# Kernel optimization log

Hardware: AMD Instinct MI355X
Metric: run time of the kernel (lower is better)

Reference implementation:

```python
import jax, jax.numpy as jnp
import numpy as np

N = 50000
E = 600000
C = 128          # out_channels (== in_channels)
L = 3            # num_conv layers
HID = 32
NUM_CLASSES = 7


def setup_inputs() -> dict:
    key = jax.random.key(0)
    ks = jax.random.split(key, 16)
    bound = 1.0 / np.sqrt(C)
    inp = {
        "x": jax.random.normal(ks[0], (N, C), dtype=jnp.float32),
        "edge_index": jax.random.randint(ks[1], (2, E), 0, N, dtype=jnp.int32),
        "edge_weight": jax.random.uniform(ks[2], (E,), dtype=jnp.float32),
        # GatedGraphConv weight: [num_layers, C, C], uniform(-1/sqrt(C), 1/sqrt(C))
        "conv_weight": jax.random.uniform(ks[3], (L, C, C), minval=-bound, maxval=bound, dtype=jnp.float32),
        # GRUCell params (torch layout: [3C, C] for ih and hh, gate order r,z,n)
        "w_ih": jax.random.uniform(ks[4], (3 * C, C), minval=-bound, maxval=bound, dtype=jnp.float32),
        "w_hh": jax.random.uniform(ks[5], (3 * C, C), minval=-bound, maxval=bound, dtype=jnp.float32),
        "b_ih": jax.random.uniform(ks[6], (3 * C,), minval=-bound, maxval=bound, dtype=jnp.float32),
        "b_hh": jax.random.uniform(ks[7], (3 * C,), minval=-bound, maxval=bound, dtype=jnp.float32),
        # MLP: C -> 32 -> 32 -> 32 -> NUM_CLASSES, tanh between hidden layers
        "w0": jax.random.normal(ks[8], (HID, C), dtype=jnp.float32) * 0.05,
        "b0": jnp.zeros((HID,), dtype=jnp.float32),
        "w1": jax.random.normal(ks[9], (HID, HID), dtype=jnp.float32) * 0.1,
        "b1": jnp.zeros((HID,), dtype=jnp.float32),
        "w2": jax.random.normal(ks[10], (HID, HID), dtype=jnp.float32) * 0.1,
        "b2": jnp.zeros((HID,), dtype=jnp.float32),
        "w3": jax.random.normal(ks[11], (NUM_CLASSES, HID), dtype=jnp.float32) * 0.1,
        "b3": jnp.zeros((NUM_CLASSES,), dtype=jnp.float32),
    }
    return inp


def _gru_cell(m, h, w_ih, w_hh, b_ih, b_hh):
    # torch GRUCell: gates ordered (r, z, n)
    gx = m @ w_ih.T + b_ih          # [N, 3C]
    gh = h @ w_hh.T + b_hh          # [N, 3C]
    xr, xz, xn = jnp.split(gx, 3, axis=-1)
    hr, hz, hn = jnp.split(gh, 3, axis=-1)
    r = jax.nn.sigmoid(xr + hr)
    z = jax.nn.sigmoid(xz + hz)
    n = jnp.tanh(xn + r * hn)
    return (1.0 - z) * n + z * h


def reference(x, edge_index, edge_weight, conv_weight, w_ih, w_hh, b_ih, b_hh,
              w0, b0, w1, b1, w2, b2, w3, b3):
    src, dst = edge_index[0], edge_index[1]
    h = x  # in_channels == out_channels, no padding needed
    for i in range(L):
        m = h @ conv_weight[i]                          # [N, C] dense GEMM
        msgs = edge_weight[:, None] * m[src]            # gather + edge weighting [E, C]
        agg = jax.ops.segment_sum(msgs, dst, num_segments=N)  # scatter-add [N, C]
        h = _gru_cell(agg, h, w_ih, w_hh, b_ih, b_hh)
    # MLP with tanh between hidden layers, linear last
    y = jnp.tanh(h @ w0.T + b0)
    y = jnp.tanh(y @ w1.T + b1)
    y = jnp.tanh(y @ w2.T + b2)
    y = y @ w3.T + b3
    return jax.nn.log_softmax(y, axis=-1)
```

## Files before the change

kernel.cpp:

```cpp
#include <hip/hip_runtime.h>
#include <hip/hip_bf16.h>
#include <math.h>

#define NN 50000
#define NE 600000
#define CC 128
#define NL 3
#define NRG (NN / 16)
#define C_RG 4
#define G_RG 4
#define SCAN_B 196

typedef __attribute__((ext_vector_type(8))) short bf16x8;
typedef __attribute__((ext_vector_type(4))) float f32x4;
typedef unsigned short ushort_t;
typedef unsigned int uint_t;

__device__ inline ushort_t f2bf(float f) {
    __hip_bfloat16 b = __float2bfloat16(f);
    return *reinterpret_cast<ushort_t*>(&b);
}
__device__ inline float bf2f(ushort_t u) {
    return __uint_as_float(((uint_t)u) << 16);
}
__device__ inline float fsig(float x) {
    return __builtin_amdgcn_rcpf(1.f + __builtin_amdgcn_exp2f(-1.44269504f * x));
}
__device__ inline float ftanh(float x) {
    float e = __builtin_amdgcn_exp2f(2.88539008f * fabsf(x));
    float t = 1.f - 2.f * __builtin_amdgcn_rcpf(e + 1.f);
    return copysignf(t, x);
}

__global__ __launch_bounds__(256) void k_cvt(const float* __restrict__ x,
                                             ushort_t* __restrict__ h_bf) {
    size_t i = (size_t)blockIdx.x * 256 + threadIdx.x;
    float4 v = ((const float4*)x)[i];
    ushort4 u;
    u.x = f2bf(v.x); u.y = f2bf(v.y); u.z = f2bf(v.z); u.w = f2bf(v.w);
    ((ushort4*)h_bf)[i] = u;
}

__global__ __launch_bounds__(256) void k_wpack(const float* __restrict__ W,
                                               ushort_t* __restrict__ pk) {
    int tid = blockIdx.x * 256 + threadIdx.x;
    int e = tid & 7;
    int l = (tid >> 3) & 63;
    int s = (tid >> 9) & 3;
    int rest = tid >> 11;
    int g = rest % 3, c0 = rest / 3;
    int row = g * 128 + c0 * 16 + (l & 15);
    int col = s * 32 + (l >> 4) * 8 + e;
    pk[tid] = f2bf(W[row * 128 + col]);
}

__global__ __launch_bounds__(256) void k_cpack(const float* __restrict__ cw,
                                               ushort_t* __restrict__ pk) {
    int tid = blockIdx.x * 256 + threadIdx.x;
    int e = tid & 7;
    int l = (tid >> 3) & 63;
    int s = (tid >> 9) & 3;
    int rest = tid >> 11;
    int c0 = rest & 7, layer = rest >> 3;
    int c = c0 * 16 + (l & 15);
    int k = s * 32 + (l >> 4) * 8 + e;
    pk[tid] = f2bf(cw[layer * 16384 + k * 128 + c]);
}

__global__ __launch_bounds__(256) void k_mpack(const float* __restrict__ w0,
                                               const float* __restrict__ w1,
                                               const float* __restrict__ w2,
                                               const float* __restrict__ w3,
                                               ushort_t* __restrict__ pk) {
    int tid = blockIdx.x * 256 + threadIdx.x;
    if (tid >= 6656) return;
    int e = tid & 7;
    int l = (tid >> 3) & 63;
    int lr = l & 15, lg = l >> 4;
    if (tid < 4096) {
        int s = (tid >> 9) & 3;
        int c0 = tid >> 11;
        pk[tid] = f2bf(w0[(c0 * 16 + lr) * 128 + s * 32 + lg * 8 + e]);
    } else if (tid < 5120) {
        int c0 = (tid - 4096) >> 9;
        pk[tid] = f2bf(w1[(c0 * 16 + lr) * 32 + lg * 8 + e]);
    } else if (tid < 6144) {
        int c0 = (tid - 5120) >> 9;
        pk[tid] = f2bf(w2[(c0 * 16 + lr) * 32 + lg * 8 + e]);
    } else {
        pk[tid] = (lr < 7) ? f2bf(w3[lr * 32 + lg * 8 + e]) : (ushort_t)0;
    }
}

__global__ __launch_bounds__(256) void k_count(const int* __restrict__ dst,
                                               int* __restrict__ deg) {
    int e = blockIdx.x * 256 + threadIdx.x;
    if (e < NE) atomicAdd(&deg[dst[e]], 1);
}

__global__ __launch_bounds__(256) void k_scan1(const int* __restrict__ deg,
                                               int* __restrict__ off,
                                               int* __restrict__ bsum) {
    __shared__ int sm[256];
    int t = threadIdx.x, i = blockIdx.x * 256 + t;
    int v = (i < NN) ? deg[i] : 0;
    sm[t] = v;
    __syncthreads();
#pragma unroll
    for (int ofs = 1; ofs < 256; ofs <<= 1) {
        int u = (t >= ofs) ? sm[t - ofs] : 0;
        __syncthreads();
        sm[t] += u;
        __syncthreads();
    }
    if (i < NN) off[i] = sm[t] - v;
    if (t == 255) bsum[blockIdx.x] = sm[255];
}

__global__ __launch_bounds__(256) void k_scan2(const int* __restrict__ bsum,
                                               int* __restrict__ bofs,
                                               int* __restrict__ off) {
    __shared__ int sm[256];
    int t = threadIdx.x;
    int v = (t < SCAN_B) ? bsum[t] : 0;
    sm[t] = v;
    __syncthreads();
#pragma unroll
    for (int ofs = 1; ofs < 256; ofs <<= 1) {
        int u = (t >= ofs) ? sm[t - ofs] : 0;
        __syncthreads();
        sm[t] += u;
        __syncthreads();
    }
    if (t < SCAN_B) bofs[t] = sm[t] - v;
    if (t == 255) off[NN] = sm[255];
}

__global__ __launch_bounds__(256) void k_scan3(int* __restrict__ off,
                                               const int* __restrict__ bofs,
                                               int* __restrict__ cursor) {
    int t = threadIdx.x, i = blockIdx.x * 256 + t;
    if (i < NN) {
        int o = off[i] + bofs[blockIdx.x];
        off[i] = o;
        cursor[i] = o;
    }
}

__global__ __launch_bounds__(256) void k_fill(const int* __restrict__ src,
                                              const int* __restrict__ dst,
                                              const float* __restrict__ ew,
                                              int* __restrict__ cursor,
                                              uint2* __restrict__ e_pair) {
    int e = blockIdx.x * 256 + threadIdx.x;
    if (e >= NE) return;
    int d = dst[e];
    int p = atomicAdd(&cursor[d], 1);
    uint2 pr;
    pr.x = (uint_t)src[e];
    pr.y = __float_as_uint(ew[e]);
    e_pair[p] = pr;
}

__global__ __launch_bounds__(256, 2) void k_conv(const ushort_t* __restrict__ h_bf,
                                                 const ushort_t* __restrict__ cw_pk,
                                                 ushort_t* __restrict__ m_bf) {
    int wid = (blockIdx.x * 256 + threadIdx.x) >> 6;
    int l = threadIdx.x & 63;
    int lr = l & 15, lg = l >> 4;
    int c0g = wid & 3;
    int chunk = wid >> 2;

    bf16x8 B[2][4];
    {
        const bf16x8* pw = (const bf16x8*)cw_pk;
#pragma unroll
        for (int p = 0; p < 2; p++)
#pragma unroll
            for (int s = 0; s < 4; s++)
                B[p][s] = pw[(size_t)(((c0g + 4 * p) * 4 + s) * 64) + l];
    }
    int c_lo = c0g * 16 + lr;

    for (int it = 0; it < C_RG; it++) {
        int rg = chunk * C_RG + it;
        if (rg >= NRG) break;
        int n0 = rg * 16;
        const short* ap = (const short*)h_bf + (size_t)(n0 + lr) * CC + lg * 8;
        bf16x8 a[4];
#pragma unroll
        for (int s = 0; s < 4; s++) a[s] = *(const bf16x8*)(ap + s * 32);
        f32x4 acc0 = {0.f,0.f,0.f,0.f}, acc1 = {0.f,0.f,0.f,0.f};
#pragma unroll
        for (int s = 0; s < 4; s++) {
            acc0 = __builtin_amdgcn_mfma_f32_16x16x32_bf16(a[s], B[0][s], acc0, 0, 0, 0);
            acc1 = __builtin_amdgcn_mfma_f32_16x16x32_bf16(a[s], B[1][s], acc1, 0, 0, 0);
        }
#pragma unroll
        for (int j = 0; j < 4; j++) {
            size_t row = (size_t)(n0 + lg * 4 + j) * CC;
            m_bf[row + c_lo] = f2bf(acc0[j]);
            m_bf[row + c_lo + 64] = f2bf(acc1[j]);
        }
    }
}

__global__ __launch_bounds__(256) void k_agg(const int* __restrict__ off,
                                             const uint2* __restrict__ e_pair,
                                             const ushort_t* __restrict__ m_bf,
                                             ushort_t* __restrict__ agg_bf) {
    int node = blockIdx.x * 4 + (threadIdx.x >> 6);
    int l = threadIdx.x & 63;
    int half = l >> 5, sl = l & 31;
    if (node >= NN) return;
    int b = off[node], e = off[node + 1];
    const uint2* m2 = (const uint2*)m_bf;
    float a0 = 0.f, a1 = 0.f, a2 = 0.f, a3 = 0.f;
    int i = b;
    for (; i + 4 <= e; i += 4) {
        uint2 p0 = e_pair[i + half];
        uint2 p1 = e_pair[i + 2 + half];
        uint2 v0 = m2[(size_t)p0.x * 32 + sl];
        uint2 v1 = m2[(size_t)p1.x * 32 + sl];
        float w0 = __uint_as_float(p0.y), w1 = __uint_as_float(p1.y);
        a0 += w0 * bf2f((ushort_t)(v0.x & 0xffffu)) + w1 * bf2f((ushort_t)(v1.x & 0xffffu));
        a1 += w0 * bf2f((ushort_t)(v0.x >> 16))     + w1 * bf2f((ushort_t)(v1.x >> 16));
        a2 += w0 * bf2f((ushort_t)(v0.y & 0xffffu)) + w1 * bf2f((ushort_t)(v1.y & 0xffffu));
        a3 += w0 * bf2f((ushort_t)(v0.y >> 16))     + w1 * bf2f((ushort_t)(v1.y >> 16));
    }
    for (; i < e; i += 2) {
        int idx = i + half;
        uint2 pr = (idx < e) ? e_pair[idx] : make_uint2(0u, 0u);
        uint2 v = m2[(size_t)pr.x * 32 + sl];
        float w = __uint_as_float(pr.y);
        a0 += w * bf2f((ushort_t)(v.x & 0xffffu));
        a1 += w * bf2f((ushort_t)(v.x >> 16));
        a2 += w * bf2f((ushort_t)(v.y & 0xffffu));
        a3 += w * bf2f((ushort_t)(v.y >> 16));
    }
    a0 += __shfl_xor(a0, 32);
    a1 += __shfl_xor(a1, 32);
    a2 += __shfl_xor(a2, 32);
    a3 += __shfl_xor(a3, 32);
    if (half == 0) {
        uint2 p;
        p.x = (uint_t)f2bf(a0) | ((uint_t)f2bf(a1) << 16);
        p.y = (uint_t)f2bf(a2) | ((uint_t)f2bf(a3) << 16);
        ((uint2*)agg_bf)[(size_t)node * 32 + sl] = p;
    }
}

__global__ __launch_bounds__(256, 2) void k_gru(const ushort_t* __restrict__ agg_bf,
                                                const ushort_t* __restrict__ hbf_in,
                                                ushort_t* __restrict__ hbf_out,
                                                const ushort_t* __restrict__ wx_pk,
                                                const ushort_t* __restrict__ wh_pk,
                                                const float* __restrict__ b_ih,
                                                const float* __restrict__ b_hh) {
    int wid = (blockIdx.x * 256 + threadIdx.x) >> 6;
    int l = threadIdx.x & 63;
    int c0 = wid & 7;
    int chunk = wid >> 3;
    int lr = l & 15, lg = l >> 4;

    bf16x8 BX[12], BH[12];
    {
        const bf16x8* px = (const bf16x8*)wx_pk + (size_t)c0 * 12 * 64 + l;
        const bf16x8* ph = (const bf16x8*)wh_pk + (size_t)c0 * 12 * 64 + l;
#pragma unroll
        for (int f = 0; f < 12; f++) { BX[f] = px[f * 64]; BH[f] = ph[f * 64]; }
    }
    int c = c0 * 16 + lr;
    float bxr = b_ih[c], bxz = b_ih[128 + c], bxn = b_ih[256 + c];
    float bhr = b_hh[c], bhz = b_hh[128 + c], bhn = b_hh[256 + c];

    for (int it = 0; it < G_RG; it++) {
        int rg = chunk * G_RG + it;
        if (rg >= NRG) break;
        int n0 = rg * 16;
        const short* ap = (const short*)agg_bf + (size_t)(n0 + lr) * CC + lg * 8;
        const short* hp = (const short*)hbf_in + (size_t)(n0 + lr) * CC + lg * 8;
        bf16x8 a[4], hf[4];
#pragma unroll
        for (int s = 0; s < 4; s++) {
            a[s] = *(const bf16x8*)(ap + s * 32);
            hf[s] = *(const bf16x8*)(hp + s * 32);
        }
        float hv[4];
#pragma unroll
        for (int j = 0; j < 4; j++)
            hv[j] = bf2f(hbf_in[(size_t)(n0 + lg * 4 + j) * CC + c]);

        f32x4 r0 = {0.f,0.f,0.f,0.f}, r1 = {0.f,0.f,0.f,0.f}, r2 = {0.f,0.f,0.f,0.f};
        f32x4 r3 = {0.f,0.f,0.f,0.f}, r4 = {0.f,0.f,0.f,0.f}, r5 = {0.f,0.f,0.f,0.f};
#pragma unroll
        for (int s = 0; s < 4; s++) {
            r0 = __builtin_amdgcn_mfma_f32_16x16x32_bf16(a[s], BX[s], r0, 0, 0, 0);
            r1 = __builtin_amdgcn_mfma_f32_16x16x32_bf16(a[s], BX[4 + s], r1, 0, 0, 0);
            r2 = __builtin_amdgcn_mfma_f32_16x16x32_bf16(a[s], BX[8 + s], r2, 0, 0, 0);
            r3 = __builtin_amdgcn_mfma_f32_16x16x32_bf16(hf[s], BH[s], r3, 0, 0, 0);
            r4 = __builtin_amdgcn_mfma_f32_16x16x32_bf16(hf[s], BH[4 + s], r4, 0, 0, 0);
            r5 = __builtin_amdgcn_mfma_f32_16x16x32_bf16(hf[s], BH[8 + s], r5, 0, 0, 0);
        }
#pragma unroll
        for (int j = 0; j < 4; j++) {
            size_t row = (size_t)(n0 + lg * 4 + j);
            float rg_ = fsig(r0[j] + bxr + r3[j] + bhr);
            float zg = fsig(r1[j] + bxz + r4[j] + bhz);
            float ng = ftanh(r2[j] + bxn + rg_ * (r5[j] + bhn));
            float hn2 = (1.f - zg) * ng + zg * hv[j];
            hbf_out[row * CC + c] = f2bf(hn2);
        }
    }
}

__global__ __launch_bounds__(256, 2) void k_mlp(const ushort_t* __restrict__ hbf,
                                                const ushort_t* __restrict__ wm_pk,
                                                const float* __restrict__ b0,
                                                const float* __restrict__ b1,
                                                const float* __restrict__ b2,
                                                const float* __restrict__ b3,
                                                float* __restrict__ out) {
    __shared__ short vt[4][16][40];
    __shared__ float yt[4][16][8];
    int wid = (blockIdx.x * 256 + threadIdx.x) >> 6;
    int wq = threadIdx.x >> 6;
    int l = threadIdx.x & 63;
    int lr = l & 15, lg = l >> 4;

    bf16x8 W0[2][4], W1[2], W2[2], W3;
    {
        const bf16x8* pw = (const bf16x8*)wm_pk;
#pragma unroll
        for (int c0 = 0; c0 < 2; c0++)
#pragma unroll
            for (int s = 0; s < 4; s++) W0[c0][s] = pw[(c0 * 4 + s) * 64 + l];
#pragma unroll
        for (int c0 = 0; c0 < 2; c0++) {
            W1[c0] = pw[512 + c0 * 64 + l];
            W2[c0] = pw[640 + c0 * 64 + l];
        }
        W3 = pw[768 + l];
    }
    float b0v[2] = {b0[lr], b0[16 + lr]};
    float b1v[2] = {b1[lr], b1[16 + lr]};
    float b2v[2] = {b2[lr], b2[16 + lr]};
    float b3v = (lr < 7) ? b3[lr] : 0.f;

    if (wid >= NRG) return;
    int n0 = wid * 16;

    bf16x8 a[4];
    {
        const short* ap = (const short*)hbf + (size_t)(n0 + lr) * CC + lg * 8;
#pragma unroll
        for (int s = 0; s < 4; s++) a[s] = *(const bf16x8*)(ap + s * 32);
    }
#pragma unroll
    for (int c0 = 0; c0 < 2; c0++) {
        f32x4 acc = {0.f, 0.f, 0.f, 0.f};
#pragma unroll
        for (int s = 0; s < 4; s++)
            acc = __builtin_amdgcn_mfma_f32_16x16x32_bf16(a[s], W0[c0][s], acc, 0, 0, 0);
#pragma unroll
        for (int j = 0; j < 4; j++)
            vt[wq][lg * 4 + j][c0 * 16 + lr] = (short)f2bf(ftanh(acc[j] + b0v[c0]));
    }
    {
        bf16x8 av = *(const bf16x8*)&vt[wq][lr][lg * 8];
        f32x4 acc[2];
#pragma unroll
        for (int c0 = 0; c0 < 2; c0++) {
            f32x4 z = {0.f, 0.f, 0.f, 0.f};
            acc[c0] = __builtin_amdgcn_mfma_f32_16x16x32_bf16(av, W1[c0], z, 0, 0, 0);
        }
#pragma unroll
        for (int c0 = 0; c0 < 2; c0++)
#pragma unroll
            for (int j = 0; j < 4; j++)
                vt[wq][lg * 4 + j][c0 * 16 + lr] = (short)f2bf(ftanh(acc[c0][j] + b1v[c0]));
    }
    {
        bf16x8 av = *(const bf16x8*)&vt[wq][lr][lg * 8];
        f32x4 acc[2];
#pragma unroll
        for (int c0 = 0; c0 < 2; c0++) {
            f32x4 z = {0.f, 0.f, 0.f, 0.f};
            acc[c0] = __builtin_amdgcn_mfma_f32_16x16x32_bf16(av, W2[c0], z, 0, 0, 0);
        }
#pragma unroll
        for (int c0 = 0; c0 < 2; c0++)
#pragma unroll
            for (int j = 0; j < 4; j++)
                vt[wq][lg * 4 + j][c0 * 16 + lr] = (short)f2bf(ftanh(acc[c0][j] + b2v[c0]));
    }
    {
        bf16x8 av = *(const bf16x8*)&vt[wq][lr][lg * 8];
        f32x4 z = {0.f, 0.f, 0.f, 0.f};
        f32x4 acc = __builtin_amdgcn_mfma_f32_16x16x32_bf16(av, W3, z, 0, 0, 0);
        if (lr < 7) {
#pragma unroll
            for (int j = 0; j < 4; j++) yt[wq][lg * 4 + j][lr] = acc[j] + b3v;
        }
    }
    __builtin_amdgcn_s_waitcnt(0);
    if (l < 16) {
        float y[7];
#pragma unroll
        for (int j = 0; j < 7; j++) y[j] = yt[wq][l][j];
        float mx = y[0];
#pragma unroll
        for (int j = 1; j < 7; j++) mx = fmaxf(mx, y[j]);
        float se = 0.f;
#pragma unroll
        for (int j = 0; j < 7; j++) se += expf(y[j] - mx);
        float lse = mx + logf(se);
#pragma unroll
        for (int j = 0; j < 7; j++) out[(size_t)(n0 + l) * 7 + j] = y[j] - lse;
    }
}

extern "C" void kernel_launch(void* const* d_in, const int* in_sizes, int n_in,
                              void* d_out, int out_size, void* d_ws, size_t ws_size,
                              hipStream_t stream) {
    const float* x   = (const float*)d_in[0];
    const int*   ei  = (const int*)d_in[1];
    const float* ew  = (const float*)d_in[2];
    const float* cw  = (const float*)d_in[3];
    const float* wih = (const float*)d_in[4];
    const float* whh = (const float*)d_in[5];
    const float* bih = (const float*)d_in[6];
    const float* bhh = (const float*)d_in[7];
    const float* w0 = (const float*)d_in[8];
    const float* b0 = (const float*)d_in[9];
    const float* w1 = (const float*)d_in[10];
    const float* b1 = (const float*)d_in[11];
    const float* w2 = (const float*)d_in[12];
    const float* b2 = (const float*)d_in[13];
    const float* w3 = (const float*)d_in[14];
    const float* b3 = (const float*)d_in[15];
    float* out = (float*)d_out;

    ushort_t* hbf0  = (ushort_t*)d_ws;
    ushort_t* hbf1  = hbf0 + (size_t)NN * CC;
    ushort_t* m_bf  = hbf1 + (size_t)NN * CC;
    ushort_t* agg_bf= m_bf + (size_t)NN * CC;
    ushort_t* wx_pk = agg_bf + (size_t)NN * CC;
    ushort_t* wh_pk = wx_pk + 3 * CC * CC;
    ushort_t* cw_pk = wh_pk + 3 * CC * CC;
    ushort_t* wm_pk = cw_pk + 3 * CC * CC;
    uint2*    e_pair= (uint2*)(wm_pk + 6656);
    int*      off   = (int*)(e_pair + NE);
    int*      deg   = off + (NN + 1);
    int*      cursor= deg + NN;
    int*      bsum  = cursor + NN;
    int*      bofs  = bsum + SCAN_B;

    const int* src = ei;
    const int* dst = ei + NE;

    k_cvt<<<(NN * CC) / 1024, 256, 0, stream>>>(x, hbf0);
    k_wpack<<<192, 256, 0, stream>>>(wih, wx_pk);
    k_wpack<<<192, 256, 0, stream>>>(whh, wh_pk);
    k_cpack<<<192, 256, 0, stream>>>(cw, cw_pk);
    k_mpack<<<26, 256, 0, stream>>>(w0, w1, w2, w3, wm_pk);

    hipMemsetAsync(deg, 0, NN * sizeof(int), stream);
    k_count<<<(NE + 255) / 256, 256, 0, stream>>>(dst, deg);
    k_scan1<<<SCAN_B, 256, 0, stream>>>(deg, off, bsum);
    k_scan2<<<1, 256, 0, stream>>>(bsum, bofs, off);
    k_scan3<<<SCAN_B, 256, 0, stream>>>(off, bofs, cursor);
    k_fill<<<(NE + 255) / 256, 256, 0, stream>>>(src, dst, ew, cursor, e_pair);

    const int conv_waves = 4 * ((NRG + C_RG - 1) / C_RG);
    const int conv_blk = (conv_waves + 3) / 4;
    const int gru_waves = 8 * ((NRG + G_RG - 1) / G_RG);
    const int gru_blk = (gru_waves + 3) / 4;

    ushort_t* hin = hbf0;
    ushort_t* hout = hbf1;
    for (int l = 0; l < NL; l++) {
        k_conv<<<conv_blk, 256, 0, stream>>>(hin, cw_pk + (size_t)l * CC * CC, m_bf);
        k_agg<<<(NN + 3) / 4, 256, 0, stream>>>(off, e_pair, m_bf, agg_bf);
        k_gru<<<gru_blk, 256, 0, stream>>>(agg_bf, hin, hout, wx_pk, wh_pk, bih, bhh);
        ushort_t* tmp = hin; hin = hout; hout = tmp;
    }
    k_mlp<<<(NRG + 3) / 4, 256, 0, stream>>>(hin, wm_pk, b0, b1, b2, b3, out);
}
```

Baseline: 328.0 us.

## Merge prep kernels, vectorize degree count, bucket CSR fill, unroll aggregation

Five setup kernels plus the memset are folded into one k_prep launch to cut launch overhead. k_count now reads dst as int4. k_fill is rebuilt so each of 196 blocks scans all edges and fills only its own 256-node range, using LDS atomics instead of global cursor atomics. The aggregation loop also gains an 8-edge unrolled step for more memory-level parallelism. The new fill makes every block read the whole dst array (196x redundant reads), which could cost more than the atomics it removes.

Measured after the change: 451.4 us. 1.38x slower.

```diff
diff --git a/kernel.cpp b/kernel.cpp
--- a/kernel.cpp
+++ b/kernel.cpp
@@ -32,70 +32,96 @@
     return copysignf(t, x);
 }
 
-__global__ __launch_bounds__(256) void k_cvt(const float* __restrict__ x,
-                                             ushort_t* __restrict__ h_bf) {
-    size_t i = (size_t)blockIdx.x * 256 + threadIdx.x;
-    float4 v = ((const float4*)x)[i];
-    ushort4 u;
-    u.x = f2bf(v.x); u.y = f2bf(v.y); u.z = f2bf(v.z); u.w = f2bf(v.w);
-    ((ushort4*)h_bf)[i] = u;
-}
-
-__global__ __launch_bounds__(256) void k_wpack(const float* __restrict__ W,
-                                               ushort_t* __restrict__ pk) {
-    int tid = blockIdx.x * 256 + threadIdx.x;
-    int e = tid & 7;
-    int l = (tid >> 3) & 63;
-    int s = (tid >> 9) & 3;
-    int rest = tid >> 11;
-    int g = rest % 3, c0 = rest / 3;
-    int row = g * 128 + c0 * 16 + (l & 15);
-    int col = s * 32 + (l >> 4) * 8 + e;
-    pk[tid] = f2bf(W[row * 128 + col]);
-}
-
-__global__ __launch_bounds__(256) void k_cpack(const float* __restrict__ cw,
-                                               ushort_t* __restrict__ pk) {
-    int tid = blockIdx.x * 256 + threadIdx.x;
-    int e = tid & 7;
-    int l = (tid >> 3) & 63;
-    int s = (tid >> 9) & 3;
-    int rest = tid >> 11;
-    int c0 = rest & 7, layer = rest >> 3;
-    int c = c0 * 16 + (l & 15);
-    int k = s * 32 + (l >> 4) * 8 + e;
-    pk[tid] = f2bf(cw[layer * 16384 + k * 128 + c]);
-}
-
-__global__ __launch_bounds__(256) void k_mpack(const float* __restrict__ w0,
-                                               const float* __restrict__ w1,
-                                               const float* __restrict__ w2,
-                                               const float* __restrict__ w3,
-                                               ushort_t* __restrict__ pk) {
-    int tid = blockIdx.x * 256 + threadIdx.x;
-    if (tid >= 6656) return;
-    int e = tid & 7;
-    int l = (tid >> 3) & 63;
-    int lr = l & 15, lg = l >> 4;
-    if (tid < 4096) {
+__global__ __launch_bounds__(256) void k_prep(const float* __restrict__ x,
+                                              ushort_t* __restrict__ h_bf,
+                                              const float* __restrict__ wih,
+                                              const float* __restrict__ whh,
+                                              const float* __restrict__ cw,
+                                              const float* __restrict__ w0,
+                                              const float* __restrict__ w1,
+                                              const float* __restrict__ w2,
+                                              const float* __restrict__ w3,
+                                              ushort_t* __restrict__ wx_pk,
+                                              ushort_t* __restrict__ wh_pk,
+                                              ushort_t* __restrict__ cw_pk,
+                                              ushort_t* __restrict__ wm_pk,
+                                              int* __restrict__ deg) {
+    int bid = blockIdx.x;
+    int t = threadIdx.x;
+    if (bid < 6250) {
+        size_t i = (size_t)bid * 256 + t;
+        float4 v = ((const float4*)x)[i];
+        ushort4 u;
+        u.x = f2bf(v.x); u.y = f2bf(v.y); u.z = f2bf(v.z); u.w = f2bf(v.w);
+        ((ushort4*)h_bf)[i] = u;
+        return;
+    }
+    int bb = bid - 6250;
+    if (bb < 384) {
+        const float* W = (bb < 192) ? wih : whh;
+        ushort_t* pk = (bb < 192) ? wx_pk : wh_pk;
+        int tid = ((bb < 192) ? bb : bb - 192) * 256 + t;
+        int e = tid & 7;
+        int l = (tid >> 3) & 63;
         int s = (tid >> 9) & 3;
-        int c0 = tid >> 11;
-        pk[tid] = f2bf(w0[(c0 * 16 + lr) * 128 + s * 32 + lg * 8 + e]);
-    } else if (tid < 5120) {
-        int c0 = (tid - 4096) >> 9;
-        pk[tid] = f2bf(w1[(c0 * 16 + lr) * 32 + lg * 8 + e]);
-    } else if (tid < 6144) {
-        int c0 = (tid - 5120) >> 9;
-        pk[tid] = f2bf(w2[(c0 * 16 + lr) * 32 + lg * 8 + e]);
-    } else {
-        pk[tid] = (lr < 7) ? f2bf(w3[lr * 32 + lg * 8 + e]) : (ushort_t)0;
+        int rest = tid >> 11;
+        int g = rest % 3, c0 = rest / 3;
+        int row = g * 128 + c0 * 16 + (l & 15);
+        int col = s * 32 + (l >> 4) * 8 + e;
+        pk[tid] = f2bf(W[row * 128 + col]);
+        return;
+    }
+    bb -= 384;
+    if (bb < 192) {
+        int tid = bb * 256 + t;
+        int e = tid & 7;
+        int l = (tid >> 3) & 63;
+        int s = (tid >> 9) & 3;
+        int rest = tid >> 11;
+        int c0 = rest & 7, layer = rest >> 3;
+        int c = c0 * 16 + (l & 15);
+        int k = s * 32 + (l >> 4) * 8 + e;
+        cw_pk[tid] = f2bf(cw[layer * 16384 + k * 128 + c]);
+        return;
+    }
+    bb -= 192;
+    if (bb < 26) {
+        int tid = bb * 256 + t;
+        if (tid >= 6656) return;
+        int e = tid & 7;
+        int l = (tid >> 3) & 63;
+        int lr = l & 15, lg = l >> 4;
+        if (tid < 4096) {
+            int s = (tid >> 9) & 3;
+            int c0 = tid >> 11;
+            wm_pk[tid] = f2bf(w0[(c0 * 16 + lr) * 128 + s * 32 + lg * 8 + e]);
+        } else if (tid < 5120) {
+            int c0 = (tid - 4096) >> 9;
+            wm_pk[tid] = f2bf(w1[(c0 * 16 + lr) * 32 + lg * 8 + e]);
+        } else if (tid < 6144) {
+            int c0 = (tid - 5120) >> 9;
+            wm_pk[tid] = f2bf(w2[(c0 * 16 + lr) * 32 + lg * 8 + e]);
+        } else {
+            wm_pk[tid] = (lr < 7) ? f2bf(w3[lr * 32 + lg * 8 + e]) : (ushort_t)0;
+        }
+        return;
+    }
+    bb -= 26;
+    {
+        int i = bb * 256 + t;
+        if (i < NN) deg[i] = 0;
     }
 }
 
 __global__ __launch_bounds__(256) void k_count(const int* __restrict__ dst,
                                                int* __restrict__ deg) {
-    int e = blockIdx.x * 256 + threadIdx.x;
-    if (e < NE) atomicAdd(&deg[dst[e]], 1);
+    int c = blockIdx.x * 256 + threadIdx.x;
+    if (c >= NE / 4) return;
+    int4 d4 = ((const int4*)dst)[c];
+    atomicAdd(&deg[d4.x], 1);
+    atomicAdd(&deg[d4.y], 1);
+    atomicAdd(&deg[d4.z], 1);
+    atomicAdd(&deg[d4.w], 1);
 }
 
 __global__ __launch_bounds__(256) void k_scan1(const int* __restrict__ deg,
@@ -137,29 +163,39 @@
 }
 
 __global__ __launch_bounds__(256) void k_scan3(int* __restrict__ off,
-                                               const int* __restrict__ bofs,
-                                               int* __restrict__ cursor) {
-    int t = threadIdx.x, i = blockIdx.x * 256 + t;
-    if (i < NN) {
-        int o = off[i] + bofs[blockIdx.x];
-        off[i] = o;
-        cursor[i] = o;
-    }
-}
-
-__global__ __launch_bounds__(256) void k_fill(const int* __restrict__ src,
+                                               const int* __restrict__ bofs) {
+    int i = blockIdx.x * 256 + threadIdx.x;
+    if (i < NN) off[i] += bofs[blockIdx.x];
+}
+
+__global__ __launch_bounds__(512) void k_fill(const int* __restrict__ src,
                                               const int* __restrict__ dst,
                                               const float* __restrict__ ew,
-                                              int* __restrict__ cursor,
+                                              const int* __restrict__ off,
                                               uint2* __restrict__ e_pair) {
-    int e = blockIdx.x * 256 + threadIdx.x;
-    if (e >= NE) return;
-    int d = dst[e];
-    int p = atomicAdd(&cursor[d], 1);
-    uint2 pr;
-    pr.x = (uint_t)src[e];
-    pr.y = __float_as_uint(ew[e]);
-    e_pair[p] = pr;
+    __shared__ int lcur[256];
+    int t = threadIdx.x;
+    int base = blockIdx.x * 256;
+    if (t < 256) lcur[t] = 0;
+    __syncthreads();
+    const int4* dst4 = (const int4*)dst;
+    for (int c = t; c < NE / 4; c += 512) {
+        int4 d4 = dst4[c];
+        int e0 = c * 4;
+        int dd[4] = {d4.x, d4.y, d4.z, d4.w};
+#pragma unroll
+        for (int q = 0; q < 4; q++) {
+            int r = dd[q] - base;
+            if ((unsigned)r < 256u) {
+                int lp = atomicAdd(&lcur[r], 1);
+                int p = off[dd[q]] + lp;
+                uint2 pr;
+                pr.x = (uint_t)src[e0 + q];
+                pr.y = __float_as_uint(ew[e0 + q]);
+                e_pair[p] = pr;
+            }
+        }
+    }
 }
 
 __global__ __launch_bounds__(256, 2) void k_conv(const ushort_t* __restrict__ h_bf,
@@ -217,6 +253,26 @@
     const uint2* m2 = (const uint2*)m_bf;
     float a0 = 0.f, a1 = 0.f, a2 = 0.f, a3 = 0.f;
     int i = b;
+    for (; i + 8 <= e; i += 8) {
+        uint2 p0 = e_pair[i + half];
+        uint2 p1 = e_pair[i + 2 + half];
+        uint2 p2 = e_pair[i + 4 + half];
+        uint2 p3 = e_pair[i + 6 + half];
+        uint2 v0 = m2[(size_t)p0.x * 32 + sl];
+        uint2 v1 = m2[(size_t)p1.x * 32 + sl];
+        uint2 v2 = m2[(size_t)p2.x * 32 + sl];
+        uint2 v3 = m2[(size_t)p3.x * 32 + sl];
+        float w0 = __uint_as_float(p0.y), w1 = __uint_as_float(p1.y);
+        float w2 = __uint_as_float(p2.y), w3 = __uint_as_float(p3.y);
+        a0 += w0 * bf2f((ushort_t)(v0.x & 0xffffu)) + w1 * bf2f((ushort_t)(v1.x & 0xffffu))
+            + w2 * bf2f((ushort_t)(v2.x & 0xffffu)) + w3 * bf2f((ushort_t)(v3.x & 0xffffu));
+        a1 += w0 * bf2f((ushort_t)(v0.x >> 16))     + w1 * bf2f((ushort_t)(v1.x >> 16))
+            + w2 * bf2f((ushort_t)(v2.x >> 16))     + w3 * bf2f((ushort_t)(v3.x >> 16));
+        a2 += w0 * bf2f((ushort_t)(v0.y & 0xffffu)) + w1 * bf2f((ushort_t)(v1.y & 0xffffu))
+            + w2 * bf2f((ushort_t)(v2.y & 0xffffu)) + w3 * bf2f((ushort_t)(v3.y & 0xffffu));
+        a3 += w0 * bf2f((ushort_t)(v0.y >> 16))     + w1 * bf2f((ushort_t)(v1.y >> 16))
+            + w2 * bf2f((ushort_t)(v2.y >> 16))     + w3 * bf2f((ushort_t)(v3.y >> 16));
+    }
     for (; i + 4 <= e; i += 4) {
         uint2 p0 = e_pair[i + half];
         uint2 p1 = e_pair[i + 2 + half];
@@ -452,25 +508,20 @@
     uint2*    e_pair= (uint2*)(wm_pk + 6656);
     int*      off   = (int*)(e_pair + NE);
     int*      deg   = off + (NN + 1);
-    int*      cursor= deg + NN;
-    int*      bsum  = cursor + NN;
+    int*      bsum  = deg + NN;
     int*      bofs  = bsum + SCAN_B;
 
     const int* src = ei;
     const int* dst = ei + NE;
 
-    k_cvt<<<(NN * CC) / 1024, 256, 0, stream>>>(x, hbf0);
-    k_wpack<<<192, 256, 0, stream>>>(wih, wx_pk);
-    k_wpack<<<192, 256, 0, stream>>>(whh, wh_pk);
-    k_cpack<<<192, 256, 0, stream>>>(cw, cw_pk);
-    k_mpack<<<26, 256, 0, stream>>>(w0, w1, w2, w3, wm_pk);
-
-    hipMemsetAsync(deg, 0, NN * sizeof(int), stream);
-    k_count<<<(NE + 255) / 256, 256, 0, stream>>>(dst, deg);
+    k_prep<<<7048, 256, 0, stream>>>(x, hbf0, wih, whh, cw, w0, w1, w2, w3,
+                                     wx_pk, wh_pk, cw_pk, wm_pk, deg);
+
+    k_count<<<(NE / 4 + 255) / 256, 256, 0, stream>>>(dst, deg);
     k_scan1<<<SCAN_B, 256, 0, stream>>>(deg, off, bsum);
     k_scan2<<<1, 256, 0, stream>>>(bsum, bofs, off);
-    k_scan3<<<SCAN_B, 256, 0, stream>>>(off, bofs, cursor);
-    k_fill<<<(NE + 255) / 256, 256, 0, stream>>>(src, dst, ew, cursor, e_pair);
+    k_scan3<<<SCAN_B, 256, 0, stream>>>(off, bofs);
+    k_fill<<<SCAN_B, 512, 0, stream>>>(src, dst, ew, off, e_pair);
 
     const int conv_waves = 4 * ((NRG + C_RG - 1) / C_RG);
     const int conv_blk = (conv_waves + 3) / 4;
```
